# Kernel optimization log

Hardware: AMD Instinct MI355X
Metric: run time of the kernel (lower is better)

Reference implementation:

```python
import jax, jax.numpy as jnp
import numpy as np

N = 50000          # nodes
E_RAND = 250000    # random edges (self-loops appended -> E = 300000)
MARKER, OUT = 20, 16
FEAT = MARKER * OUT        # 320
T1, T2, T3 = 1.0, 5.0, 0.1
BN_EPS = 1e-5


def setup_inputs() -> dict:
    key = jax.random.key(0)
    k0, k1, k2, k3 = jax.random.split(key, 4)
    x = jax.random.normal(k0, (N, FEAT), jnp.float32)
    loops = jnp.arange(N, dtype=jnp.int32)
    src = jnp.concatenate([jax.random.randint(k1, (E_RAND,), 0, N, jnp.int32), loops])
    dst = jnp.concatenate([jax.random.randint(k2, (E_RAND,), 0, N, jnp.int32), loops])
    return {
        "x": x,
        "src": src,
        "dst": dst,
        "marker_weight": jnp.ones((MARKER, OUT), jnp.float32),
        "bn_weight": jnp.ones((OUT,), jnp.float32),
        "bn_bias": jnp.zeros((OUT,), jnp.float32),
        "ref_center": jax.random.normal(k3, (OUT, FEAT), jnp.float32),
        "beta": jnp.ones((1,), jnp.float32),
    }


def agnn_conv(h, src, dst, beta, temp):
    """AGNNConv: cosine edge scores, edge softmax over dst, weighted scatter-sum."""
    norm = jnp.sqrt(jnp.sum(h * h, axis=-1, keepdims=True))
    nh = h / jnp.maximum(norm, 1e-12)                 # F.normalize(p=2, eps=1e-12)
    cos = jnp.sum(nh[src] * nh[dst], axis=-1)         # per-edge dot product [E]
    e = (beta[0] * cos) / temp
    # numerically stable edge softmax segmented by destination node
    emax = jax.ops.segment_max(e, dst, num_segments=N)
    ex = jnp.exp(e - emax[dst])
    esum = jax.ops.segment_sum(ex, dst, num_segments=N)
    attn = ex / esum[dst]                             # [E]
    # weighted aggregation of (unnormalized) source features
    return jax.ops.segment_sum(h[src] * attn[:, None], dst, num_segments=N)


def reference(x, src, dst, marker_weight, bn_weight, bn_bias, ref_center, beta):
    fea = agnn_conv(x, src, dst, beta, T1)
    fea = agnn_conv(fea, src, dst, beta, T1)
    fea = fea.reshape(-1, MARKER, OUT) * marker_weight[None]   # MarkerWeight
    f = fea.sum(axis=1)                                        # [N, OUT]
    fea = fea.reshape(-1, MARKER * OUT)
    # BatchNorm1d (training mode: batch stats, biased variance)
    mean = f.mean(axis=0)
    var = f.var(axis=0)
    f = (f - mean) / jnp.sqrt(var + BN_EPS) * bn_weight + bn_bias
    f = jnp.where(f >= 0, f, 0.25 * f)                         # LeakyReLU(0.25)
    p = jax.nn.softmax(f / T3, axis=1) @ ref_center            # RefCentroid
    out = agnn_conv(f, src, dst, beta, T1)
    out = agnn_conv(out, src, dst, beta, T1)
    out = jax.nn.softmax(out / T2, axis=1)
    return (fea, f, p, out)
```

## Files before the change

### kernel.cpp

```cpp
#include <hip/hip_runtime.h>
#include <hip/hip_fp16.h>
#include <cstdint>
#include <cstddef>


#define D_BIG 320

__device__ __forceinline__ float dot4(float4 a, float4 b) {
    return a.x * b.x + a.y * b.y + a.z * b.z + a.w * b.w;
}

union h4u { uint2 u; __half2 h[2]; };

__device__ __forceinline__ float4 h4_to_f4(uint2 raw) {
    h4u pk; pk.u = raw;
    float2 lo = __half22float2(pk.h[0]);
    float2 hi = __half22float2(pk.h[1]);
    return float4{lo.x, lo.y, hi.x, hi.y};
}

__device__ __forceinline__ uint2 f4_to_h4(float4 v) {
    h4u pk;
    pk.h[0] = __floats2half2_rn(v.x, v.y);
    pk.h[1] = __floats2half2_rn(v.z, v.w);
    return pk.u;
}

__global__ void fill_u32(unsigned* p, unsigned v, int n) {
    int i = blockIdx.x * blockDim.x + threadIdx.x;
    if (i < n) p[i] = v;
}

__global__ void count_deg(const int* __restrict__ dst, unsigned* __restrict__ deg, int nE) {
    int k = blockIdx.x * blockDim.x + threadIdx.x;
    if (k < nE) atomicAdd(&deg[dst[k]], 1u);
}

__global__ void scan1(const unsigned* __restrict__ deg, unsigned* __restrict__ rs,
                      unsigned* __restrict__ bsum, int n) {
    __shared__ unsigned buf[256];
    int i = blockIdx.x * 256 + threadIdx.x;
    unsigned v = (i < n) ? deg[i] : 0u;
    buf[threadIdx.x] = v;
    __syncthreads();
    for (int off = 1; off < 256; off <<= 1) {
        unsigned t = (threadIdx.x >= (unsigned)off) ? buf[threadIdx.x - off] : 0u;
        __syncthreads();
        buf[threadIdx.x] += t;
        __syncthreads();
    }
    if (i < n) rs[i] = buf[threadIdx.x] - v;
    if (threadIdx.x == 255) bsum[blockIdx.x] = buf[255];
}

__global__ void scan2(unsigned* __restrict__ bsum, int nb) {
    __shared__ unsigned buf[256];
    unsigned v = ((int)threadIdx.x < nb) ? bsum[threadIdx.x] : 0u;
    buf[threadIdx.x] = v;
    __syncthreads();
    for (int off = 1; off < 256; off <<= 1) {
        unsigned t = (threadIdx.x >= (unsigned)off) ? buf[threadIdx.x - off] : 0u;
        __syncthreads();
        buf[threadIdx.x] += t;
        __syncthreads();
    }
    if ((int)threadIdx.x < nb) bsum[threadIdx.x] = buf[threadIdx.x] - v;
}

__global__ void scan3(unsigned* __restrict__ rs, const unsigned* __restrict__ bsum,
                      unsigned* __restrict__ cursor, float* __restrict__ stats,
                      int n, int nE) {
    int i = blockIdx.x * 256 + threadIdx.x;
    if (i < n) { rs[i] += bsum[blockIdx.x]; cursor[i] = 0u; }
    if (i == 0) rs[n] = (unsigned)nE;
    if (blockIdx.x == 0 && threadIdx.x < 64) stats[threadIdx.x] = 0.f;
}

__global__ void scatter_edges(const int* __restrict__ src, const int* __restrict__ dst,
                              const unsigned* __restrict__ rowstart, unsigned* __restrict__ cursor,
                              int* __restrict__ esrc, int nE) {
    int k = blockIdx.x * blockDim.x + threadIdx.x;
    if (k >= nE) return;
    int t = dst[k];
    unsigned pos = rowstart[t] + atomicAdd(&cursor[t], 1u);
    esrc[pos] = src[k];
}

__global__ void hist_block(const unsigned* __restrict__ deg, unsigned* __restrict__ blockhist,
                           int n, int nb) {
    __shared__ unsigned lh[64];
    if (threadIdx.x < 64) lh[threadIdx.x] = 0u;
    __syncthreads();
    int i = blockIdx.x * 256 + threadIdx.x;
    if (i < n) atomicAdd(&lh[min(deg[i], 63u)], 1u);
    __syncthreads();
    if (threadIdx.x < 64) blockhist[threadIdx.x * nb + blockIdx.x] = lh[threadIdx.x];
}

__global__ void scan_buckets(unsigned* __restrict__ blockhist, unsigned* __restrict__ btot, int nb) {
    __shared__ unsigned buf[256];
    int b = blockIdx.x;
    int k = threadIdx.x;
    unsigned v = (k < nb) ? blockhist[b * nb + k] : 0u;
    buf[k] = v;
    __syncthreads();
    for (int off = 1; off < 256; off <<= 1) {
        unsigned t = (k >= off) ? buf[k - off] : 0u;
        __syncthreads();
        buf[k] += t;
        __syncthreads();
    }
    if (k < nb) blockhist[b * nb + k] = buf[k] - v;
    if (k == 255) btot[b] = buf[255];
}

__global__ void scan_hist(unsigned* __restrict__ hist) {
    int t = threadIdx.x;
    unsigned v = hist[t];
    unsigned p = v;
    #pragma unroll
    for (int off = 1; off < 64; off <<= 1) {
        unsigned o = __shfl_up(p, off, 64);
        if (t >= off) p += o;
    }
    hist[t] = p - v;
}

__global__ void place2(const unsigned* __restrict__ deg, const unsigned* __restrict__ blockhist,
                       const unsigned* __restrict__ bbase, int* __restrict__ perm,
                       int n, int nb) {
    __shared__ unsigned lc[64];
    if (threadIdx.x < 64) lc[threadIdx.x] = 0u;
    __syncthreads();
    int i = blockIdx.x * 256 + threadIdx.x;
    if (i < n) {
        unsigned bin  = min(deg[i], 63u);
        unsigned rank = atomicAdd(&lc[bin], 1u);
        unsigned pos  = bbase[bin] + blockhist[bin * nb + blockIdx.x] + rank;
        perm[pos] = i;
    }
}

__global__ void prep_x(const float* __restrict__ x, uint2* __restrict__ xh,
                       float* __restrict__ invn, int n) {
    int g    = (blockIdx.x * blockDim.x + threadIdx.x) >> 4;
    int lane = threadIdx.x & 15;
    if (g >= n) return;
    const float4* p = (const float4*)(x + (size_t)g * D_BIG);
    uint2* ph = xh + (size_t)g * 80;
    float s2 = 0.f;
    #pragma unroll
    for (int q = 0; q < 5; q++) {
        float4 v = p[lane + 16 * q];
        s2 += dot4(v, v);
        ph[lane + 16 * q] = f4_to_h4(v);
    }
    #pragma unroll
    for (int m = 8; m >= 1; m >>= 1) s2 += __shfl_xor(s2, m, 16);
    if (lane == 0) invn[g] = 1.f / fmaxf(sqrtf(s2), 1e-12f);
}

template <int EPI>
__global__ void agnn_big(const uint2* __restrict__ h,
                         const unsigned* __restrict__ rowstart,
                         const int* __restrict__ esrc,
                         const int* __restrict__ perm,
                         const float* __restrict__ beta,
                         const float* __restrict__ inv_in,
                         const float* __restrict__ mw,
                         float* __restrict__ out,
                         uint2* __restrict__ out_h,
                         float* __restrict__ inv_out,
                         float* __restrict__ f_out,
                         int n) {
    int g    = (blockIdx.x * blockDim.x + threadIdx.x) >> 4;
    int lane = threadIdx.x & 15;
    if (g >= n) return;
    int node = perm[g];
    unsigned r0 = rowstart[node], r1 = rowstart[node + 1];
    float b0 = beta[0];
    float M  = fabsf(b0);
    float bs = b0 * inv_in[node];

    const uint2* pd = h + (size_t)node * 80;
    float4 d[5];
    #pragma unroll
    for (int q = 0; q < 5; q++) d[q] = h4_to_f4(pd[lane + 16 * q]);

    float4 a[5];
    #pragma unroll
    for (int q = 0; q < 5; q++) a[q] = float4{0.f, 0.f, 0.f, 0.f};
    float lrun = 0.f;

    for (unsigned base = r0; base < r1; base += 16) {
        unsigned j = base + (unsigned)lane;
        bool  vld = j < r1;
        int   sv  = vld ? esrc[j] : 0;
        float iv  = vld ? inv_in[sv] : 0.f;
        int cnt = (int)min(r1 - base, 16u);
        for (int t = 0; t < cnt; t++) {
            int   s   = __shfl(sv, t, 16);
            float ins = __shfl(iv, t, 16);
            const uint2* ps = h + (size_t)s * 80;
            float4 r[5];
            #pragma unroll
            for (int q = 0; q < 5; q++) r[q] = h4_to_f4(ps[lane + 16 * q]);
            float dt = 0.f;
            #pragma unroll
            for (int q = 0; q < 5; q++) dt += dot4(r[q], d[q]);
            #pragma unroll
            for (int m = 8; m >= 1; m >>= 1) dt += __shfl_xor(dt, m, 16);
            float w = __expf(bs * ins * dt - M);
            lrun += w;
            #pragma unroll
            for (int q = 0; q < 5; q++) {
                a[q].x += w * r[q].x; a[q].y += w * r[q].y;
                a[q].z += w * r[q].z; a[q].w += w * r[q].w;
            }
        }
    }
    float inv = 1.f / lrun;
    #pragma unroll
    for (int q = 0; q < 5; q++) { a[q].x *= inv; a[q].y *= inv; a[q].z *= inv; a[q].w *= inv; }

    if (EPI == 0) {
        uint2* po = out_h + (size_t)node * 80;
        #pragma unroll
        for (int q = 0; q < 5; q++) po[lane + 16 * q] = f4_to_h4(a[q]);
        float s2 = 0.f;
        #pragma unroll
        for (int q = 0; q < 5; q++) s2 += dot4(a[q], a[q]);
        #pragma unroll
        for (int m = 8; m >= 1; m >>= 1) s2 += __shfl_xor(s2, m, 16);
        if (lane == 0) inv_out[node] = 1.f / fmaxf(sqrtf(s2), 1e-12f);
    } else {
        const float4* pmw = (const float4*)mw;
        float4 v[5];
        #pragma unroll
        for (int q = 0; q < 5; q++) {
            float4 wq = pmw[lane + 16 * q];
            v[q] = float4{a[q].x * wq.x, a[q].y * wq.y, a[q].z * wq.z, a[q].w * wq.w};
        }
        float4* po = (float4*)(out + (size_t)node * D_BIG);
        #pragma unroll
        for (int q = 0; q < 5; q++) po[lane + 16 * q] = v[q];
        float fs0 = v[0].x + v[1].x + v[2].x + v[3].x + v[4].x;
        float fs1 = v[0].y + v[1].y + v[2].y + v[3].y + v[4].y;
        float fs2 = v[0].z + v[1].z + v[2].z + v[3].z + v[4].z;
        float fs3 = v[0].w + v[1].w + v[2].w + v[3].w + v[4].w;
        #pragma unroll
        for (int m = 4; m <= 8; m <<= 1) {
            fs0 += __shfl_xor(fs0, m, 16);
            fs1 += __shfl_xor(fs1, m, 16);
            fs2 += __shfl_xor(fs2, m, 16);
            fs3 += __shfl_xor(fs3, m, 16);
        }
        if (lane < 4)
            ((float4*)(f_out + (size_t)node * 16))[lane] = float4{fs0, fs1, fs2, fs3};
    }
}

template <int EPI>
__global__ void agnn_small(const float* __restrict__ h,
                           const unsigned* __restrict__ rowstart,
                           const int* __restrict__ esrc,
                           const int* __restrict__ perm,
                           const float* __restrict__ beta,
                           const float* __restrict__ inv_in,
                           float* __restrict__ out,
                           float* __restrict__ inv_out,
                           float inv_temp,
                           int n) {
    int g    = (blockIdx.x * blockDim.x + threadIdx.x) >> 4;
    int lane = threadIdx.x & 15;
    if (g >= n) return;
    int node = perm[g];
    unsigned r0 = rowstart[node], r1 = rowstart[node + 1];
    float b0 = beta[0];
    float M  = fabsf(b0);
    float bs = b0 * inv_in[node];

    float dv = h[(size_t)node * 16 + lane];
    float acc = 0.f, lrun = 0.f;

    for (unsigned base = r0; base < r1; base += 16) {
        unsigned j = base + (unsigned)lane;
        bool  vld = j < r1;
        int   sv  = vld ? esrc[j] : 0;
        float iv  = vld ? inv_in[sv] : 0.f;
        int cnt = (int)min(r1 - base, 16u);
        for (int t = 0; t < cnt; t++) {
            int   s   = __shfl(sv, t, 16);
            float ins = __shfl(iv, t, 16);
            float rv = h[(size_t)s * 16 + lane];
            float dt = rv * dv;
            #pragma unroll
            for (int m = 8; m >= 1; m >>= 1) dt += __shfl_xor(dt, m, 16);
            float w = __expf(bs * ins * dt - M);
            lrun += w;
            acc += w * rv;
        }
    }
    float val = acc / lrun;

    if (EPI == 0) {
        out[(size_t)node * 16 + lane] = val;
        float s2 = val * val;
        #pragma unroll
        for (int m = 8; m >= 1; m >>= 1) s2 += __shfl_xor(s2, m, 16);
        if (lane == 0) inv_out[node] = 1.f / fmaxf(sqrtf(s2), 1e-12f);
    } else {
        float v2 = val * inv_temp;
        float mx = v2;
        #pragma unroll
        for (int m = 8; m >= 1; m >>= 1) mx = fmaxf(mx, __shfl_xor(mx, m, 16));
        float ee = __expf(v2 - mx);
        float ss = ee;
        #pragma unroll
        for (int m = 8; m >= 1; m >>= 1) ss += __shfl_xor(ss, m, 16);
        out[(size_t)node * 16 + lane] = ee / ss;
    }
}

__global__ void bn_reduce(const float* __restrict__ f, float* __restrict__ stats, int n) {
    int c = threadIdx.x & 15;
    int g = threadIdx.x >> 4;
    float s = 0.f, s2 = 0.f;
    for (int i = blockIdx.x * 16 + g; i < n; i += gridDim.x * 16) {
        float v = f[(size_t)i * 16 + c];
        s += v; s2 += v * v;
    }
    __shared__ float ls[256], ls2[256];
    ls[threadIdx.x] = s; ls2[threadIdx.x] = s2;
    __syncthreads();
    for (int off = 128; off >= 16; off >>= 1) {
        if ((int)threadIdx.x < off) {
            ls[threadIdx.x]  += ls[threadIdx.x + off];
            ls2[threadIdx.x] += ls2[threadIdx.x + off];
        }
        __syncthreads();
    }
    if (threadIdx.x < 16) {
        atomicAdd(&stats[threadIdx.x], ls[threadIdx.x]);
        atomicAdd(&stats[16 + threadIdx.x], ls2[threadIdx.x]);
    }
}

__global__ void bn_finalize(float* __restrict__ stats, const float* __restrict__ w,
                            const float* __restrict__ b, int n) {
    int c = threadIdx.x;
    if (c < 16) {
        float mean  = stats[c] / (float)n;
        float var   = fmaxf(stats[16 + c] / (float)n - mean * mean, 0.f);
        float scale = w[c] / sqrtf(var + 1e-5f);
        stats[32 + c] = scale;
        stats[48 + c] = b[c] - mean * scale;
    }
}

__global__ void __launch_bounds__(256)
bn_apply_p(float* __restrict__ f, const float* __restrict__ stats,
           const float* __restrict__ rc, float* __restrict__ p,
           float* __restrict__ invf, int n) {
    __shared__ float s_sc[16], s_sh[16];
    if (threadIdx.x < 16) { s_sc[threadIdx.x] = stats[32 + threadIdx.x]; s_sh[threadIdx.x] = stats[48 + threadIdx.x]; }
    __syncthreads();

    int lane = threadIdx.x & 63;

    float rcw[16][5];
    #pragma unroll
    for (int c = 0; c < 16; c++) {
        #pragma unroll
        for (int u = 0; u < 5; u++) rcw[c][u] = rc[c * D_BIG + lane + 64 * u];
    }

    int wave = (blockIdx.x * blockDim.x + threadIdx.x) >> 6;
    int nw   = (gridDim.x * blockDim.x) >> 6;

    for (int i = wave; i < n; i += nw) {
        const float* fr = f + (size_t)i * 16;
        float fv[16];
        float mx = -1e30f;
        #pragma unroll
        for (int c = 0; c < 16; c++) {
            float v = fmaf(fr[c], s_sc[c], s_sh[c]);
            v = (v >= 0.f) ? v : 0.25f * v;
            fv[c] = v;
            mx = fmaxf(mx, v);
        }
        if (lane < 16) {
            float v = fmaf(fr[lane], s_sc[lane], s_sh[lane]);
            v = (v >= 0.f) ? v : 0.25f * v;
            f[(size_t)i * 16 + lane] = v;
        }

        float s2 = 0.f;
        #pragma unroll
        for (int c = 0; c < 16; c++) s2 += fv[c] * fv[c];
        if (lane == 0) invf[i] = 1.f / fmaxf(sqrtf(s2), 1e-12f);

        float sp[16]; float sum = 0.f;
        #pragma unroll
        for (int c = 0; c < 16; c++) { float t = __expf((fv[c] - mx) * 10.0f); sp[c] = t; sum += t; }
        float isum = 1.f / sum;

        #pragma unroll
        for (int u = 0; u < 5; u++) {
            float acc0 = 0.f, acc1 = 0.f;
            #pragma unroll
            for (int c = 0; c < 16; c += 2) {
                acc0 = fmaf(sp[c],     rcw[c][u],     acc0);
                acc1 = fmaf(sp[c + 1], rcw[c + 1][u], acc1);
            }
            p[(size_t)i * D_BIG + lane + 64 * u] = (acc0 + acc1) * isum;
        }
    }
}

extern "C" void kernel_launch(void* const* d_in, const int* in_sizes, int n_in,
                              void* d_out, int out_size, void* d_ws, size_t ws_size,
                              hipStream_t stream) {
    const float* x    = (const float*)d_in[0];
    const int*   src  = (const int*)d_in[1];
    const int*   dst  = (const int*)d_in[2];
    const float* mw   = (const float*)d_in[3];
    const float* bnw  = (const float*)d_in[4];
    const float* bnb  = (const float*)d_in[5];
    const float* rc   = (const float*)d_in[6];
    const float* beta = (const float*)d_in[7];

    const int n  = in_sizes[0] / D_BIG;
    const int nE = in_sizes[1];

    float* out     = (float*)d_out;
    float* fea_out = out;
    float* f_out   = out + (size_t)n * D_BIG;
    float* p_out   = f_out + (size_t)n * 16;
    float* o_out   = p_out + (size_t)n * D_BIG;

    uint2* xh  = (uint2*)fea_out;
    uint2* h1h = (uint2*)p_out;

    const int TB = 256;
    auto cdiv = [](int a, int b) { return (a + b - 1) / b; };
    const int nb   = cdiv(n, 256);
    const int ngrp = cdiv(n, 16);

    char* w = (char*)d_ws;
    auto carve = [&](size_t bytes) { void* r = (void*)w; w += (bytes + 255) & ~(size_t)255; return r; };
    unsigned* deg       = (unsigned*)carve((size_t)n * 4);
    unsigned* rowstart  = (unsigned*)carve((size_t)(n + 1) * 4);
    unsigned* cursor    = (unsigned*)carve((size_t)n * 4);
    unsigned* bsum      = (unsigned*)carve(256 * 4);
    int*      esrc      = (int*)carve((size_t)nE * 4);
    float*    stats     = (float*)carve(64 * 4);
    float*    t16       = (float*)carve((size_t)n * 16 * 4);
    int*      perm      = (int*)carve((size_t)n * 4);
    unsigned* blockhist = (unsigned*)carve((size_t)64 * nb * 4);
    unsigned* btot      = (unsigned*)carve(64 * 4);
    float*    inv_x     = (float*)carve((size_t)n * 4);
    float*    inv_h1    = (float*)carve((size_t)n * 4);
    float*    inv_f     = (float*)carve((size_t)n * 4);
    float*    inv_t     = (float*)carve((size_t)n * 4);

    fill_u32<<<cdiv(n, TB), TB, 0, stream>>>(deg, 0u, n);
    count_deg<<<cdiv(nE, TB), TB, 0, stream>>>(dst, deg, nE);
    scan1<<<nb, 256, 0, stream>>>(deg, rowstart, bsum, n);
    scan2<<<1, 256, 0, stream>>>(bsum, nb);
    scan3<<<nb, 256, 0, stream>>>(rowstart, bsum, cursor, stats, n, nE);
    scatter_edges<<<cdiv(nE, TB), TB, 0, stream>>>(src, dst, rowstart, cursor, esrc, nE);

    hist_block<<<nb, 256, 0, stream>>>(deg, blockhist, n, nb);
    scan_buckets<<<64, 256, 0, stream>>>(blockhist, btot, nb);
    scan_hist<<<1, 64, 0, stream>>>(btot);
    place2<<<nb, 256, 0, stream>>>(deg, blockhist, btot, perm, n, nb);

    prep_x<<<ngrp, TB, 0, stream>>>(x, xh, inv_x, n);
    agnn_big<0><<<ngrp, TB, 0, stream>>>(xh, rowstart, esrc, perm, beta, inv_x,
                                         nullptr, nullptr, h1h, inv_h1, nullptr, n);
    agnn_big<1><<<ngrp, TB, 0, stream>>>(h1h, rowstart, esrc, perm, beta, inv_h1,
                                         mw, fea_out, nullptr, nullptr, f_out, n);
    bn_reduce<<<128, TB, 0, stream>>>(f_out, stats, n);
    bn_finalize<<<1, 16, 0, stream>>>(stats, bnw, bnb, n);
    bn_apply_p<<<1024, TB, 0, stream>>>(f_out, stats, rc, p_out, inv_f, n);
    agnn_small<0><<<ngrp, TB, 0, stream>>>(f_out, rowstart, esrc, perm, beta, inv_f,
                                           t16, inv_t, 0.f, n);
    agnn_small<2><<<ngrp, TB, 0, stream>>>(t16, rowstart, esrc, perm, beta, inv_t,
                                           o_out, nullptr, 0.2f, n);
}
```

Measured before the change: 392.5 us.

## Prefetch next neighbor row in AGNN loops, fuse degree histogram into scan, sort descending

The AGNN gather loops in both the big and small kernels now load the next source node's feature row before processing the current one. This software pipelining is meant to hide gather latency behind the dot, exp and accumulate work. The per-block degree histogram is folded into scan1, which removes one kernel launch and one extra read of deg. Bins are reversed so nodes are ordered by descending degree, putting high-degree nodes first to reduce tail imbalance. The cost is more registers for the prefetch buffer, which may lower occupancy in the big kernel.

After: 378.9 us. -3.5%, faster.

```diff
diff --git a/kernel.cpp b/kernel.cpp
--- a/kernel.cpp
+++ b/kernel.cpp
@@ -37,12 +37,16 @@
 }
 
 __global__ void scan1(const unsigned* __restrict__ deg, unsigned* __restrict__ rs,
-                      unsigned* __restrict__ bsum, int n) {
+                      unsigned* __restrict__ bsum, unsigned* __restrict__ blockhist,
+                      int n, int nb) {
     __shared__ unsigned buf[256];
+    __shared__ unsigned lh[64];
+    if (threadIdx.x < 64) lh[threadIdx.x] = 0u;
     int i = blockIdx.x * 256 + threadIdx.x;
     unsigned v = (i < n) ? deg[i] : 0u;
     buf[threadIdx.x] = v;
     __syncthreads();
+    if (i < n) atomicAdd(&lh[63u - min(v, 63u)], 1u);
     for (int off = 1; off < 256; off <<= 1) {
         unsigned t = (threadIdx.x >= (unsigned)off) ? buf[threadIdx.x - off] : 0u;
         __syncthreads();
@@ -51,6 +55,8 @@
     }
     if (i < n) rs[i] = buf[threadIdx.x] - v;
     if (threadIdx.x == 255) bsum[blockIdx.x] = buf[255];
+    __syncthreads();
+    if (threadIdx.x < 64) blockhist[threadIdx.x * nb + blockIdx.x] = lh[threadIdx.x];
 }
 
 __global__ void scan2(unsigned* __restrict__ bsum, int nb) {
@@ -86,17 +92,6 @@
     esrc[pos] = src[k];
 }
 
-__global__ void hist_block(const unsigned* __restrict__ deg, unsigned* __restrict__ blockhist,
-                           int n, int nb) {
-    __shared__ unsigned lh[64];
-    if (threadIdx.x < 64) lh[threadIdx.x] = 0u;
-    __syncthreads();
-    int i = blockIdx.x * 256 + threadIdx.x;
-    if (i < n) atomicAdd(&lh[min(deg[i], 63u)], 1u);
-    __syncthreads();
-    if (threadIdx.x < 64) blockhist[threadIdx.x * nb + blockIdx.x] = lh[threadIdx.x];
-}
-
 __global__ void scan_buckets(unsigned* __restrict__ blockhist, unsigned* __restrict__ btot, int nb) {
     __shared__ unsigned buf[256];
     int b = blockIdx.x;
@@ -134,7 +129,7 @@
     __syncthreads();
     int i = blockIdx.x * 256 + threadIdx.x;
     if (i < n) {
-        unsigned bin  = min(deg[i], 63u);
+        unsigned bin  = 63u - min(deg[i], 63u);
         unsigned rank = atomicAdd(&lc[bin], 1u);
         unsigned pos  = bbase[bin] + blockhist[bin * nb + blockIdx.x] + rank;
         perm[pos] = i;
@@ -198,13 +193,26 @@
         int   sv  = vld ? esrc[j] : 0;
         float iv  = vld ? inv_in[sv] : 0.f;
         int cnt = (int)min(r1 - base, 16u);
+        int s0 = __shfl(sv, 0, 16);
+        const uint2* ps0 = h + (size_t)s0 * 80;
+        uint2 rn[5];
+        #pragma unroll
+        for (int q = 0; q < 5; q++) rn[q] = ps0[lane + 16 * q];
+
         for (int t = 0; t < cnt; t++) {
-            int   s   = __shfl(sv, t, 16);
+            uint2 rcur[5];
+            #pragma unroll
+            for (int q = 0; q < 5; q++) rcur[q] = rn[q];
+            if (t + 1 < cnt) {
+                int s1 = __shfl(sv, t + 1, 16);
+                const uint2* ps1 = h + (size_t)s1 * 80;
+                #pragma unroll
+                for (int q = 0; q < 5; q++) rn[q] = ps1[lane + 16 * q];
+            }
             float ins = __shfl(iv, t, 16);
-            const uint2* ps = h + (size_t)s * 80;
             float4 r[5];
             #pragma unroll
-            for (int q = 0; q < 5; q++) r[q] = h4_to_f4(ps[lane + 16 * q]);
+            for (int q = 0; q < 5; q++) r[q] = h4_to_f4(rcur[q]);
             float dt = 0.f;
             #pragma unroll
             for (int q = 0; q < 5; q++) dt += dot4(r[q], d[q]);
@@ -289,10 +297,15 @@
         int   sv  = vld ? esrc[j] : 0;
         float iv  = vld ? inv_in[sv] : 0.f;
         int cnt = (int)min(r1 - base, 16u);
+        int s0 = __shfl(sv, 0, 16);
+        float rv_next = h[(size_t)s0 * 16 + lane];
         for (int t = 0; t < cnt; t++) {
-            int   s   = __shfl(sv, t, 16);
+            float rv = rv_next;
+            if (t + 1 < cnt) {
+                int s1 = __shfl(sv, t + 1, 16);
+                rv_next = h[(size_t)s1 * 16 + lane];
+            }
             float ins = __shfl(iv, t, 16);
-            float rv = h[(size_t)s * 16 + lane];
             float dt = rv * dv;
             #pragma unroll
             for (int m = 8; m >= 1; m >>= 1) dt += __shfl_xor(dt, m, 16);
@@ -466,12 +479,11 @@
 
     fill_u32<<<cdiv(n, TB), TB, 0, stream>>>(deg, 0u, n);
     count_deg<<<cdiv(nE, TB), TB, 0, stream>>>(dst, deg, nE);
-    scan1<<<nb, 256, 0, stream>>>(deg, rowstart, bsum, n);
+    scan1<<<nb, 256, 0, stream>>>(deg, rowstart, bsum, blockhist, n, nb);
     scan2<<<1, 256, 0, stream>>>(bsum, nb);
     scan3<<<nb, 256, 0, stream>>>(rowstart, bsum, cursor, stats, n, nE);
     scatter_edges<<<cdiv(nE, TB), TB, 0, stream>>>(src, dst, rowstart, cursor, esrc, nE);
 
-    hist_block<<<nb, 256, 0, stream>>>(deg, blockhist, n, nb);
     scan_buckets<<<64, 256, 0, stream>>>(blockhist, btot, nb);
     scan_hist<<<1, 64, 0, stream>>>(btot);
     place2<<<nb, 256, 0, stream>>>(deg, blockhist, btot, perm, n, nb);
```
